# Kernel optimization log

Hardware: AMD Instinct MI355X
Metric: run time of the kernel (lower is better)

## Reference

```python
import jax, jax.numpy as jnp
from jax import lax
import numpy as np

V, D, H = 50257, 128, 256  # vocab, d_model, d_hidden
B, T = 16, 128             # batch, seq_len


def setup_inputs() -> dict:
    key = jax.random.key(0)
    k_ids, k_emb, k_wih, k_whh, k_out = jax.random.split(key, 5)
    s = 0.02
    return {
        "input_ids": jax.random.randint(k_ids, (B, T), 0, V, dtype=jnp.int64 if jax.config.jax_enable_x64 else jnp.int32),
        "embed": jax.random.normal(k_emb, (V, D), jnp.float32) * s,
        "W_ih": jax.random.normal(k_wih, (3 * H, D), jnp.float32) * s,
        "b_ih": jnp.zeros((3 * H,), jnp.float32),
        "W_hh": jax.random.normal(k_whh, (3 * H, H), jnp.float32) * s,
        "b_hh": jnp.zeros((3 * H,), jnp.float32),
        "W_out": jax.random.normal(k_out, (V, H), jnp.float32) * s,
    }


def reference(input_ids, embed, W_ih, b_ih, W_hh, b_hh, W_out):
    # Embedding lookup: [B,T,D]
    x = embed[input_ids]
    # Precompute input-side gate projections for all timesteps: [B,T,3H]
    gx_all = jnp.einsum('btd,gd->btg', x, W_ih) + b_ih

    def step(h, gx):
        # h: [B,H], gx: [B,3H]
        gh = h @ W_hh.T + b_hh  # [B,3H]
        xr, xz, xn = jnp.split(gx, 3, axis=-1)
        hr, hz, hn = jnp.split(gh, 3, axis=-1)
        r = jax.nn.sigmoid(xr + hr)
        z = jax.nn.sigmoid(xz + hz)
        n = jnp.tanh(xn + r * hn)  # PyTorch GRU: r gates the hidden projection
        h_new = (1.0 - z) * n + z * h
        return h_new, h_new

    h0 = jnp.zeros((x.shape[0], W_hh.shape[1]), x.dtype)
    _, hs = lax.scan(step, h0, jnp.swapaxes(gx_all, 0, 1))  # hs: [T,B,H]
    out = jnp.swapaxes(hs, 0, 1)  # [B,T,H]
    # LM head (no bias): [B,T,V]
    return jnp.einsum('bth,vh->btv', out, W_out)
```

## Files before the change

### kernel.cpp

```cpp
#include <hip/hip_runtime.h>
#include <hip/hip_bf16.h>

#define V   50257
#define VPAD 50304
#define DD  128
#define HH  256
#define G3  768
#define BB  16
#define TT  128

typedef _Float16 h2   __attribute__((ext_vector_type(2)));
typedef short  bf16x8 __attribute__((ext_vector_type(8)));
typedef float  f32x4  __attribute__((ext_vector_type(4)));

#if __has_builtin(__builtin_amdgcn_fdot2)
#define USE_FDOT2 1
#else
#define USE_FDOT2 0
#endif

__device__ __forceinline__ float sigmoid_(float x) { return 1.0f / (1.0f + __expf(-x)); }
__device__ __forceinline__ float tanh_(float x)    { float e = __expf(2.0f * x); return (e - 1.0f) / (e + 1.0f); }

__global__ __launch_bounds__(256) void k_embed_gx(
    const int* __restrict__ ids, const float* __restrict__ embed,
    const float* __restrict__ W_ih, const float* __restrict__ b_ih,
    float* __restrict__ gx)
{
    __shared__ float xs[8][DD];
    const int tid  = threadIdx.x;
    const int row0 = blockIdx.x * 8;

#pragma unroll
    for (int i = 0; i < 4; ++i) {
        int e = tid + i * 256;
        int r = e >> 7, k = e & 127;
        int id = ids[row0 + r];
        xs[r][k] = embed[(long)id * DD + k];
    }
    __syncthreads();

#pragma unroll
    for (int o = 0; o < 3; ++o) {
        int j = tid + o * 256;
        float bias = b_ih[j];
        float acc[8];
#pragma unroll
        for (int r = 0; r < 8; ++r) acc[r] = bias;
        const float4* wrow = (const float4*)(W_ih + (long)j * DD);
        for (int q = 0; q < 32; ++q) {
            float4 w = wrow[q];
#pragma unroll
            for (int r = 0; r < 8; ++r) {
                acc[r] += w.x * xs[r][q * 4 + 0] + w.y * xs[r][q * 4 + 1]
                        + w.z * xs[r][q * 4 + 2] + w.w * xs[r][q * 4 + 3];
            }
        }
#pragma unroll
        for (int r = 0; r < 8; ++r) gx[(long)(row0 + r) * G3 + j] = acc[r];
    }
}

__global__ __launch_bounds__(256) void k_convert_wout(
    const float* __restrict__ Wout, __hip_bfloat16* __restrict__ Wb)
{
    long base = ((long)blockIdx.x * 256 + threadIdx.x) * 8;
    const long VALID = (long)V * HH;
    union { __hip_bfloat16 b[8]; uint4 u; } pk;
    if (base < VALID) {
        float4 f0 = ((const float4*)Wout)[base / 4];
        float4 f1 = ((const float4*)Wout)[base / 4 + 1];
        pk.b[0] = __float2bfloat16(f0.x); pk.b[1] = __float2bfloat16(f0.y);
        pk.b[2] = __float2bfloat16(f0.z); pk.b[3] = __float2bfloat16(f0.w);
        pk.b[4] = __float2bfloat16(f1.x); pk.b[5] = __float2bfloat16(f1.y);
        pk.b[6] = __float2bfloat16(f1.z); pk.b[7] = __float2bfloat16(f1.w);
    } else {
        pk.u = make_uint4(0, 0, 0, 0);
    }
    *(uint4*)(Wb + base) = pk.u;
}

__global__ __launch_bounds__(512, 2) void k_gru(
    const float* __restrict__ gx, const float* __restrict__ W_hh,
    const float* __restrict__ b_hh, __hip_bfloat16* __restrict__ hout)
{
    __shared__ float    hf[HH];
    __shared__ _Float16 hh[HH];
    const int tid = threadIdx.x;
    const int b   = blockIdx.x;
    const int g   = tid >> 1;
    const int u   = tid & 1;

    h2 w[3][64];
#pragma unroll
    for (int o = 0; o < 3; ++o) {
        const float4* wr = (const float4*)(W_hh + (long)(o * 256 + g) * HH + u * 128);
#pragma unroll
        for (int q = 0; q < 32; ++q) {
            float4 f = wr[q];
            w[o][2 * q]     = h2{(_Float16)f.x, (_Float16)f.y};
            w[o][2 * q + 1] = h2{(_Float16)f.z, (_Float16)f.w};
        }
    }
    float bias[3];
#pragma unroll
    for (int o = 0; o < 3; ++o) bias[o] = b_hh[o * 256 + g];

    if (tid < HH) { hf[tid] = 0.0f; hh[tid] = (_Float16)0.0f; }
    __syncthreads();

    const float* gxrow = gx + (long)b * TT * G3;
    for (int t = 0; t < TT; ++t) {
        float gxr = gxrow[g], gxz = gxrow[256 + g], gxn = gxrow[512 + g];

        float acc0 = 0.f, acc1 = 0.f, acc2 = 0.f;
        const h2* hp = ((const h2*)hh) + u * 64;
#pragma unroll
        for (int p = 0; p < 64; ++p) {
            h2 hv = hp[p];
#if USE_FDOT2
            acc0 = __builtin_amdgcn_fdot2(w[0][p], hv, acc0, false);
            acc1 = __builtin_amdgcn_fdot2(w[1][p], hv, acc1, false);
            acc2 = __builtin_amdgcn_fdot2(w[2][p], hv, acc2, false);
#else
            float hx = (float)hv.x, hy = (float)hv.y;
            acc0 += (float)w[0][p].x * hx + (float)w[0][p].y * hy;
            acc1 += (float)w[1][p].x * hx + (float)w[1][p].y * hy;
            acc2 += (float)w[2][p].x * hx + (float)w[2][p].y * hy;
#endif
        }
        acc0 += __shfl_xor(acc0, 1);
        acc1 += __shfl_xor(acc1, 1);
        acc2 += __shfl_xor(acc2, 1);

        float r = sigmoid_(gxr + acc0 + bias[0]);
        float z = sigmoid_(gxz + acc1 + bias[1]);
        float n = tanh_(gxn + r * (acc2 + bias[2]));
        float hold = hf[g];
        float hnew = (1.0f - z) * n + z * hold;

        __syncthreads();
        if (u == 0) {
            hf[g] = hnew;
            hh[g] = (_Float16)hnew;
            hout[((long)b * TT + t) * HH + g] = __float2bfloat16(hnew);
        }
        __syncthreads();
        gxrow += G3;
    }
}

__global__ __launch_bounds__(256) void k_head(
    const __hip_bfloat16* __restrict__ Ah, const __hip_bfloat16* __restrict__ Bw,
    float* __restrict__ out)
{
    __shared__ unsigned short As[128 * 64];
    __shared__ unsigned short Bs[128 * 64];
    const int i    = threadIdx.x;
    const int wave = i >> 6, lane = i & 63;
    const int quad = lane >> 4, mr = lane & 15;
    const int m0   = blockIdx.y * 128;
    const int n0   = blockIdx.x * 128;
    const int wm0  = (wave >> 1) * 64;
    const int wn0  = (wave & 1) * 64;

    f32x4 acc[4][4];
#pragma unroll
    for (int a = 0; a < 4; ++a)
#pragma unroll
        for (int c = 0; c < 4; ++c) acc[a][c] = (f32x4){0.f, 0.f, 0.f, 0.f};

    const uint4* Ag = (const uint4*)Ah;
    const uint4* Bg = (const uint4*)Bw;
    uint4* Asv = (uint4*)As;
    uint4* Bsv = (uint4*)Bs;

    for (int ks = 0; ks < 4; ++ks) {
        __syncthreads();
#pragma unroll
        for (int q = 0; q < 4; ++q) {
            int li   = q * 256 + i;
            int row  = li >> 3, slot = li & 7;
            int chunk = slot ^ (row & 7);
            Asv[li] = Ag[(long)(m0 + row) * 32 + ks * 8 + chunk];
            Bsv[li] = Bg[(long)(n0 + row) * 32 + ks * 8 + chunk];
        }
        __syncthreads();
#pragma unroll
        for (int kk = 0; kk < 2; ++kk) {
            bf16x8 af[4], bf[4];
#pragma unroll
            for (int wmi = 0; wmi < 4; ++wmi) {
                int row  = wm0 + wmi * 16 + mr;
                int slot = (kk * 4 + quad) ^ (row & 7);
                af[wmi] = *(const bf16x8*)&As[(row * 8 + slot) * 8];
            }
#pragma unroll
            for (int wni = 0; wni < 4; ++wni) {
                int row  = wn0 + wni * 16 + mr;
                int slot = (kk * 4 + quad) ^ (row & 7);
                bf[wni] = *(const bf16x8*)&Bs[(row * 8 + slot) * 8];
            }
#pragma unroll
            for (int wmi = 0; wmi < 4; ++wmi)
#pragma unroll
                for (int wni = 0; wni < 4; ++wni)
                    acc[wmi][wni] = __builtin_amdgcn_mfma_f32_16x16x32_bf16(
                        af[wmi], bf[wni], acc[wmi][wni], 0, 0, 0);
        }
    }

#pragma unroll
    for (int wmi = 0; wmi < 4; ++wmi) {
#pragma unroll
        for (int rr = 0; rr < 4; ++rr) {
            long m = m0 + wm0 + wmi * 16 + quad * 4 + rr;
            float* orow = out + m * (long)V;
#pragma unroll
            for (int wni = 0; wni < 4; ++wni) {
                int n = n0 + wn0 + wni * 16 + mr;
                if (n < V) orow[n] = acc[wmi][wni][rr];
            }
        }
    }
}

extern "C" void kernel_launch(void* const* d_in, const int* in_sizes, int n_in,
                              void* d_out, int out_size, void* d_ws, size_t ws_size,
                              hipStream_t stream) {
    const int*   ids   = (const int*)d_in[0];
    const float* embed = (const float*)d_in[1];
    const float* W_ih  = (const float*)d_in[2];
    const float* b_ih  = (const float*)d_in[3];
    const float* W_hh  = (const float*)d_in[4];
    const float* b_hh  = (const float*)d_in[5];
    const float* W_out = (const float*)d_in[6];
    float* out = (float*)d_out;

    char* ws = (char*)d_ws;
    float*          gx  = (float*)ws;
    __hip_bfloat16* hbf = (__hip_bfloat16*)(ws + 6291456);
    __hip_bfloat16* wbf = (__hip_bfloat16*)(ws + 7340032);

    k_embed_gx<<<256, 256, 0, stream>>>(ids, embed, W_ih, b_ih, gx);
    k_convert_wout<<<6288, 256, 0, stream>>>(W_out, wbf);
    k_gru<<<16, 512, 0, stream>>>(gx, W_hh, b_hh, hbf);
    k_head<<<dim3(393, 16), 256, 0, stream>>>(hbf, wbf, out);
}
```

Before: 844.7 us.

## Double-buffer GRU hidden state, prefetch gx, and use async global-to-LDS loads in head

```diff
diff --git a/kernel.cpp b/kernel.cpp
--- a/kernel.cpp
+++ b/kernel.cpp
@@ -1,17 +1,25 @@
 #include <hip/hip_runtime.h>
 #include <hip/hip_bf16.h>
 
-#define V   50257
+#define V    50257
 #define VPAD 50304
-#define DD  128
-#define HH  256
-#define G3  768
-#define BB  16
-#define TT  128
+#define DD   128
+#define HH   256
+#define G3   768
+#define BB   16
+#define TT   128
 
 typedef _Float16 h2   __attribute__((ext_vector_type(2)));
+typedef _Float16 h8   __attribute__((ext_vector_type(8)));
 typedef short  bf16x8 __attribute__((ext_vector_type(8)));
 typedef float  f32x4  __attribute__((ext_vector_type(4)));
+
+typedef __attribute__((address_space(3))) uint4* lds_u4_t;
+typedef const __attribute__((address_space(1))) uint4* gbl_u4_t;
+
+__device__ __forceinline__ void async_copy16(const uint4* g, uint4* lds_base) {
+    __builtin_amdgcn_global_load_lds((gbl_u4_t)g, (lds_u4_t)lds_base, 16, 0, 0);
+}
 
 #if __has_builtin(__builtin_amdgcn_fdot2)
 #define USE_FDOT2 1
@@ -84,8 +92,7 @@
     const float* __restrict__ gx, const float* __restrict__ W_hh,
     const float* __restrict__ b_hh, __hip_bfloat16* __restrict__ hout)
 {
-    __shared__ float    hf[HH];
-    __shared__ _Float16 hh[HH];
+    __shared__ _Float16 hh[2][HH];
     const int tid = threadIdx.x;
     const int b   = blockIdx.x;
     const int g   = tid >> 1;
@@ -106,47 +113,68 @@
 #pragma unroll
     for (int o = 0; o < 3; ++o) bias[o] = b_hh[o * 256 + g];
 
-    if (tid < HH) { hf[tid] = 0.0f; hh[tid] = (_Float16)0.0f; }
+    if (tid < HH) hh[0][tid] = (_Float16)0.0f;
     __syncthreads();
 
     const float* gxrow = gx + (long)b * TT * G3;
+    float cxr = gxrow[g], cxz = gxrow[256 + g], cxn = gxrow[512 + g];
+    float hold = 0.0f;
+
     for (int t = 0; t < TT; ++t) {
-        float gxr = gxrow[g], gxz = gxrow[256 + g], gxn = gxrow[512 + g];
-
-        float acc0 = 0.f, acc1 = 0.f, acc2 = 0.f;
-        const h2* hp = ((const h2*)hh) + u * 64;
-#pragma unroll
-        for (int p = 0; p < 64; ++p) {
-            h2 hv = hp[p];
+        const float* nrow = gxrow + G3;
+        float nxr = nrow[g], nxz = nrow[256 + g], nxn = nrow[512 + g];
+
+        float a0a = 0.f, a0b = 0.f, a1a = 0.f, a1b = 0.f, a2a = 0.f, a2b = 0.f;
+        const h8* hp8 = ((const h8*)hh[t & 1]) + u * 16;
+#pragma unroll
+        for (int c = 0; c < 16; ++c) {
+            h8 hv = hp8[c];
+            const h2* hvp = (const h2*)&hv;
+#pragma unroll
+            for (int j = 0; j < 4; ++j) {
+                h2 hq = hvp[j];
+                int p = c * 4 + j;
 #if USE_FDOT2
-            acc0 = __builtin_amdgcn_fdot2(w[0][p], hv, acc0, false);
-            acc1 = __builtin_amdgcn_fdot2(w[1][p], hv, acc1, false);
-            acc2 = __builtin_amdgcn_fdot2(w[2][p], hv, acc2, false);
+                if (j & 1) {
+                    a0b = __builtin_amdgcn_fdot2(w[0][p], hq, a0b, false);
+                    a1b = __builtin_amdgcn_fdot2(w[1][p], hq, a1b, false);
+                    a2b = __builtin_amdgcn_fdot2(w[2][p], hq, a2b, false);
+                } else {
+                    a0a = __builtin_amdgcn_fdot2(w[0][p], hq, a0a, false);
+                    a1a = __builtin_amdgcn_fdot2(w[1][p], hq, a1a, false);
+                    a2a = __builtin_amdgcn_fdot2(w[2][p], hq, a2a, false);
+                }
 #else
-            float hx = (float)hv.x, hy = (float)hv.y;
-            acc0 += (float)w[0][p].x * hx + (float)w[0][p].y * hy;
-            acc1 += (float)w[1][p].x * hx + (float)w[1][p].y * hy;
-            acc2 += (float)w[2][p].x * hx + (float)w[2][p].y * hy;
+                float hx = (float)hq.x, hy = (float)hq.y;
+                if (j & 1) {
+                    a0b += (float)w[0][p].x * hx + (float)w[0][p].y * hy;
+                    a1b += (float)w[1][p].x * hx + (float)w[1][p].y * hy;
+                    a2b += (float)w[2][p].x * hx + (float)w[2][p].y * hy;
+                } else {
+                    a0a += (float)w[0][p].x * hx + (float)w[0][p].y * hy;
+                    a1a += (float)w[1][p].x * hx + (float)w[1][p].y * hy;
+                    a2a += (float)w[2][p].x * hx + (float)w[2][p].y * hy;
+                }
 #endif
-        }
+            }
+        }
+        float acc0 = a0a + a0b, acc1 = a1a + a1b, acc2 = a2a + a2b;
         acc0 += __shfl_xor(acc0, 1);
         acc1 += __shfl_xor(acc1, 1);
         acc2 += __shfl_xor(acc2, 1);
 
-        float r = sigmoid_(gxr + acc0 + bias[0]);
-        float z = sigmoid_(gxz + acc1 + bias[1]);
-        float n = tanh_(gxn + r * (acc2 + bias[2]));
-        float hold = hf[g];
+        float r = sigmoid_(cxr + acc0 + bias[0]);
+        float z = sigmoid_(cxz + acc1 + bias[1]);
+        float n = tanh_(cxn + r * (acc2 + bias[2]));
         float hnew = (1.0f - z) * n + z * hold;
 
+        if (u == 0) hh[(t + 1) & 1][g] = (_Float16)hnew;
+        else        hout[((long)b * TT + t) * HH + g] = __float2bfloat16(hnew);
         __syncthreads();
-        if (u == 0) {
-            hf[g] = hnew;
-            hh[g] = (_Float16)hnew;
-            hout[((long)b * TT + t) * HH + g] = __float2bfloat16(hnew);
-        }
-        __syncthreads();
-        gxrow += G3;
+
+        hold = hnew;
+        cxr = nxr; cxz = nxz; cxn = nxn;
+        gxrow = nrow;
     }
 }
 
@@ -175,17 +203,27 @@
     uint4* Asv = (uint4*)As;
     uint4* Bsv = (uint4*)Bs;
 
+    const uint4* agp[4]; const uint4* bgp[4];
+    uint4* alds[4]; uint4* blds[4];
+#pragma unroll
+    for (int c = 0; c < 4; ++c) {
+        int seg   = c * 4 + wave;
+        int row   = seg * 8 + (lane >> 3);
+        int chunk = (lane & 7) ^ (row & 7);
+        agp[c] = Ag + (long)(m0 + row) * 32 + chunk;
+        bgp[c] = Bg + (long)(n0 + row) * 32 + chunk;
+        alds[c] = Asv + seg * 64;
+        blds[c] = Bsv + seg * 64;
+    }
+
     for (int ks = 0; ks < 4; ++ks) {
         __syncthreads();
 #pragma unroll
-        for (int q = 0; q < 4; ++q) {
-            int li   = q * 256 + i;
-            int row  = li >> 3, slot = li & 7;
-            int chunk = slot ^ (row & 7);
-            Asv[li] = Ag[(long)(m0 + row) * 32 + ks * 8 + chunk];
-            Bsv[li] = Bg[(long)(n0 + row) * 32 + ks * 8 + chunk];
-        }
+        for (int c = 0; c < 4; ++c) async_copy16(agp[c] + ks * 8, alds[c]);
+#pragma unroll
+        for (int c = 0; c < 4; ++c) async_copy16(bgp[c] + ks * 8, blds[c]);
         __syncthreads();
+
 #pragma unroll
         for (int kk = 0; kk < 2; ++kk) {
             bf16x8 af[4], bf[4];
```

After: 773.7 us. 1.09x faster.
